# Performance work log

Measured on AMD Instinct MI355X. Metric: run time of the kernel, lower is better.

The kernel has to match this reference:

```python
import jax, jax.numpy as jnp
import numpy as np

# ---- static radial-bin geometry (h == w == 512) ----
H = W = 512
_y, _x = np.indices((H, W))
_center = np.array([(_x.max() - _x.min()) / 2.0, (_y.max() - _y.min()) / 2.0])
_r = np.hypot(_x - _center[0], _y - _center[1])
_r_int = _r.astype(int)
NBINS = int(_r_int.max()) + 1            # all integer radii 0..NBINS-1 are present
R_INT = jnp.asarray(_r_int.ravel())       # (H*W,) int32 bin id per pixel
COUNTS = jnp.asarray(np.bincount(_r_int.ravel(), minlength=NBINS).astype(np.float32))

EPS = 1e-8


def _get_mask(freq_ri):
    """Vectorized equivalent of PSDLoss.get_mask. freq_ri: (n,c,h,w,2).

    azimuthalAverage's sort+cumsum binning == per-integer-radius mean,
    excluding bin 0 and the last bin. The sequential np.where idx-scan in
    psd1D_circle_mask is equivalent to a gather psd_ext[r_int] because psd
    values lie in [0,1] (the only possible collision, value 1.0 at idx=1,
    rewrites bin 0 with psd_ext[1] == psd_ext[0], a no-op).
    """
    comp = (freq_ri[..., 0] + EPS) + 1j * freq_ri[..., 1]   # freq_np += 1e-8
    mag = 20.0 * jnp.log(jnp.abs(comp))                      # magnitude spectrum
    n, c, h, w = mag.shape
    flat = mag.reshape(n, c, h * w)
    seg = lambda m: jax.ops.segment_sum(m, R_INT, num_segments=NBINS)
    sums = jax.vmap(jax.vmap(seg))(flat)                     # (n,c,NBINS)
    binmean = sums / COUNTS
    psd = binmean[..., 1:NBINS - 1]                          # bins 1..NBINS-2
    pmin = psd.min(axis=-1, keepdims=True)
    pmax = psd.max(axis=-1, keepdims=True)
    psd = (psd - pmin) / (pmax - pmin)                       # normalize to [0,1]
    # extend: prepend psd[0], append 0 -> length NBINS, indexed by r_int
    zero = jnp.zeros(psd.shape[:-1] + (1,), psd.dtype)
    psd_ext = jnp.concatenate([psd[..., :1], psd, zero], axis=-1)  # (n,c,NBINS)
    mask = jnp.take(psd_ext, R_INT, axis=-1).reshape(n, c, h, w)
    return mask


def _tensor2freq(img):
    f = jnp.fft.fftshift(jnp.fft.fft2(img), axes=(2, 3))
    return jnp.stack([f.real, f.imag], axis=-1)              # (n,c,h,w,2)


def reference(pred, target):
    loss_weight = 1.0
    pred_freq = _tensor2freq(pred)
    target_freq = _tensor2freq(target)
    # norm='l2', weight='recon', matrix=None (defaults)
    tmp = pred_freq ** 2 - target_freq ** 2
    tmp = tmp[..., 0] + tmp[..., 1]
    freq_distance = tmp ** 2
    mask_all = jax.lax.stop_gradient(_get_mask(pred_freq))   # detached weight
    wmat = 1.0 - mask_all
    wmat = jnp.where(jnp.isnan(wmat), 0.0, wmat)
    wmat = jnp.clip(wmat, 0.0, 1.0)
    return jnp.mean(wmat * freq_distance) * loss_weight


def setup_inputs() -> dict:
    key = jax.random.key(0)
    k1, k2 = jax.random.split(key)
    pred = jax.random.normal(k1, (8, 3, 512, 512), dtype=jnp.float32)
    target = jax.random.normal(k2, (8, 3, 512, 512), dtype=jnp.float32)
    return {"pred": pred, "target": target}
```

## Files before the change

### kernel.cpp

```cpp
#include <hip/hip_runtime.h>
#include <math.h>

#define HW 512
#define NIMG 24
#define NB 362
#define PLANE (HW*HW)
#define NC 257
#define CP (NC*HW)
#define NG 65
#define NPB (NIMG*NG)

#define OFF_PM  0
#define OFF_PD  (NPB*NB)
#define OFF_CNT (2*NPB*NB)
#define OFF_PR  1129808
#define OFF_PIm (OFF_PR + NIMG*CP)
#define OFF_TR  (OFF_PR + 2*NIMG*CP)
#define OFF_TI  (OFF_PR + 3*NIMG*CP)

__device__ __forceinline__ int rbin_odd(float u, float v) {
    return (int)(sqrtf(fmaf(u, u, v*v)) * 0.5f);
}

__device__ __forceinline__ void cmul(float& xr, float& xi, float wr, float wi) {
    float r = xr*wr - xi*wi;
    xi = xr*wi + xi*wr;
    xr = r;
}

__device__ __forceinline__ void dft8(float ar[8], float ai[8]) {
    const float C = 0.70710678118654752440f;
    float t0r=ar[0]+ar[4], t0i=ai[0]+ai[4];
    float t1r=ar[0]-ar[4], t1i=ai[0]-ai[4];
    float t2r=ar[2]+ar[6], t2i=ai[2]+ai[6];
    float t3r=ar[2]-ar[6], t3i=ai[2]-ai[6];
    float E0r=t0r+t2r, E0i=t0i+t2i;
    float E2r=t0r-t2r, E2i=t0i-t2i;
    float E1r=t1r+t3i, E1i=t1i-t3r;
    float E3r=t1r-t3i, E3i=t1i+t3r;
    float u0r=ar[1]+ar[5], u0i=ai[1]+ai[5];
    float u1r=ar[1]-ar[5], u1i=ai[1]-ai[5];
    float u2r=ar[3]+ar[7], u2i=ai[3]+ai[7];
    float u3r=ar[3]-ar[7], u3i=ai[3]-ai[7];
    float O0r=u0r+u2r, O0i=u0i+u2i;
    float O2r=u0r-u2r, O2i=u0i-u2i;
    float O1r=u1r+u3i, O1i=u1i-u3r;
    float O3r=u1r-u3i, O3i=u1i+u3r;
    float W1r = C*(O1r+O1i), W1i = C*(O1i-O1r);
    float W2r = O2i,         W2i = -O2r;
    float W3r = C*(O3i-O3r), W3i = -C*(O3r+O3i);
    ar[0]=E0r+O0r; ai[0]=E0i+O0i;
    ar[4]=E0r-O0r; ai[4]=E0i-O0i;
    ar[1]=E1r+W1r; ai[1]=E1i+W1i;
    ar[5]=E1r-W1r; ai[5]=E1i-W1i;
    ar[2]=E2r+W2r; ai[2]=E2i+W2i;
    ar[6]=E2r-W2r; ai[6]=E2i-W2i;
    ar[3]=E3r+W3r; ai[3]=E3i+W3i;
    ar[7]=E3r-W3r; ai[7]=E3i-W3i;
}

__device__ __forceinline__ void twiddle7(float ar[8], float ai[8], float wr, float wi) {
    float pr = wr, pi = wi;
    cmul(ar[1], ai[1], pr, pi);
    #pragma unroll
    for (int k = 2; k < 8; ++k) {
        float nr = pr*wr - pi*wi;
        pi = pr*wi + pi*wr;
        pr = nr;
        cmul(ar[k], ai[k], pr, pi);
    }
}

__device__ __forceinline__ void fft512x2(float Ar[8], float Ai[8],
                                         float Br[8], float Bi[8],
                                         float* Lr, float* Li, int lane) {
    float s1, c1, s2, c2;
    int k1 = lane >> 3, b = lane & 7;
    __sincosf((float)lane * (-6.28318530717958647692f/512.0f), &s1, &c1);
    __sincosf((float)b    * (-6.28318530717958647692f/64.0f),  &s2, &c2);
    dft8(Ar, Ai); twiddle7(Ar, Ai, c1, s1);
    dft8(Br, Bi); twiddle7(Br, Bi, c1, s1);
    #pragma unroll
    for (int j = 0; j < 8; ++j) { Lr[j*68+lane] = Ar[j]; Li[j*68+lane] = Ai[j]; }
    #pragma unroll
    for (int a = 0; a < 8; ++a) { Ar[a] = Lr[k1*68+8*a+b]; Ai[a] = Li[k1*68+8*a+b]; }
    #pragma unroll
    for (int j = 0; j < 8; ++j) { Lr[j*68+lane] = Br[j]; Li[j*68+lane] = Bi[j]; }
    dft8(Ar, Ai); twiddle7(Ar, Ai, c2, s2);
    #pragma unroll
    for (int a = 0; a < 8; ++a) { Br[a] = Lr[k1*68+8*a+b]; Bi[a] = Li[k1*68+8*a+b]; }
    dft8(Br, Bi); twiddle7(Br, Bi, c2, s2);
    #pragma unroll
    for (int cc = 0; cc < 8; ++cc) {
        int ad = k1*68 + 8*cc + ((b + cc) & 7);
        Lr[ad] = Ar[cc]; Li[ad] = Ai[cc];
    }
    #pragma unroll
    for (int bb = 0; bb < 8; ++bb) {
        int ad = k1*68 + 8*b + ((bb + b) & 7);
        Ar[bb] = Lr[ad]; Ai[bb] = Li[ad];
    }
    #pragma unroll
    for (int cc = 0; cc < 8; ++cc) {
        int ad = k1*68 + 8*cc + ((b + cc) & 7);
        Lr[ad] = Br[cc]; Li[ad] = Bi[cc];
    }
    dft8(Ar, Ai);
    #pragma unroll
    for (int bb = 0; bb < 8; ++bb) {
        int ad = k1*68 + 8*b + ((bb + b) & 7);
        Br[bb] = Lr[ad]; Bi[bb] = Li[ad];
    }
    dft8(Br, Bi);
}

__global__ __launch_bounds__(256) void k_counts(int* __restrict__ counts) {
    __shared__ int cb[NB];
    int t = threadIdx.x;
    for (int j = t; j < NB; j += 256) cb[j] = 0;
    __syncthreads();
    int base = blockIdx.x * 4096;
    #pragma unroll
    for (int j = 0; j < 16; ++j) {
        int idx = base + t + j*256;
        float u = fabsf(2.0f*(float)(idx >> 9)  - 511.0f);
        float v = fabsf(2.0f*(float)(idx & 511) - 511.0f);
        atomicAdd(&cb[rbin_odd(u, v)], 1);
    }
    __syncthreads();
    for (int j = t; j < NB; j += 256) atomicAdd(&counts[j], cb[j]);
}

__global__ __launch_bounds__(256, 6) void k_rowfft(const float* __restrict__ pred,
                                                   const float* __restrict__ tgt,
                                                   float* __restrict__ ws) {
    __shared__ float smem[4672];
    int t = threadIdx.x, lane = t & 63, w = t >> 6;
    int b = blockIdx.x;
    int img = b >> 6;
    int r0 = (b & 63) << 3;
    int rA = r0 + 2*w;
    const float* pA = pred + (size_t)img*PLANE + (size_t)rA*HW;
    const float* tA = tgt  + (size_t)img*PLANE + (size_t)rA*HW;
    float arA[8], aiA[8], arB[8], aiB[8];
    #pragma unroll
    for (int j = 0; j < 8; ++j) {
        arA[j] = pA[64*j + lane];      aiA[j] = tA[64*j + lane];
        arB[j] = pA[HW + 64*j + lane]; aiB[j] = tA[HW + 64*j + lane];
    }
    float* Lr = smem + w*1088;
    float* Li = Lr + 544;
    fft512x2(arA, aiA, arB, aiB, Lr, Li, lane);
    float PrA[4], PiA[4], TrA[4], TiA[4], P256A=0.f, T256A=0.f;
    float PrB[4], PiB[4], TrB[4], TiB[4], P256B=0.f, T256B=0.f;
    #pragma unroll
    for (int d = 0; d < 8; ++d) {
        int k = (lane>>3) + ((lane&7)<<3) + (d<<6);
        Lr[k] = arA[d]; Li[k] = aiA[d];
    }
    #pragma unroll
    for (int m = 0; m < 4; ++m) {
        int kk = 64*m + lane, j2 = (512 - kk) & 511;
        float z1r = Lr[kk], z1i = Li[kk], z2r = Lr[j2], z2i = Li[j2];
        PrA[m] = 0.5f*(z1r+z2r); PiA[m] = 0.5f*(z1i-z2i);
        TrA[m] = 0.5f*(z1i+z2i); TiA[m] = 0.5f*(z2r-z1r);
    }
    if (lane == 0) { P256A = Lr[256]; T256A = Li[256]; }
    #pragma unroll
    for (int d = 0; d < 8; ++d) {
        int k = (lane>>3) + ((lane&7)<<3) + (d<<6);
        Lr[k] = arB[d]; Li[k] = aiB[d];
    }
    #pragma unroll
    for (int m = 0; m < 4; ++m) {
        int kk = 64*m + lane, j2 = (512 - kk) & 511;
        float z1r = Lr[kk], z1i = Li[kk], z2r = Lr[j2], z2i = Li[j2];
        PrB[m] = 0.5f*(z1r+z2r); PiB[m] = 0.5f*(z1i-z2i);
        TrB[m] = 0.5f*(z1i+z2i); TiB[m] = 0.5f*(z2r-z1r);
    }
    if (lane == 0) { P256B = Lr[256]; T256B = Li[256]; }

    float* TAt = smem;
    float* TBt = smem + 2336;
    __syncthreads();
    #pragma unroll
    for (int m = 0; m < 4; ++m) {
        int kk = 64*m + lane;
        TAt[kk*9 + 2*w]   = PrA[m]; TAt[kk*9 + 2*w+1] = PrB[m];
        TBt[kk*9 + 2*w]   = PiA[m]; TBt[kk*9 + 2*w+1] = PiB[m];
    }
    if (lane == 0) {
        TAt[256*9 + 2*w] = P256A; TAt[256*9 + 2*w+1] = P256B;
        TBt[256*9 + 2*w] = 0.f;   TBt[256*9 + 2*w+1] = 0.f;
    }
    __syncthreads();
    for (int idx = t; idx < 2*NC; idx += 256) {
        int comp = (idx >= NC);
        int col = idx - comp*NC;
        const float* Tt = comp ? TBt : TAt;
        float* outP = ws + (size_t)(comp ? OFF_PIm : OFF_PR)
                      + (size_t)img*CP + (size_t)col*HW + r0;
        *(float4*)outP       = make_float4(Tt[col*9],   Tt[col*9+1], Tt[col*9+2], Tt[col*9+3]);
        *(float4*)(outP + 4) = make_float4(Tt[col*9+4], Tt[col*9+5], Tt[col*9+6], Tt[col*9+7]);
    }
    __syncthreads();
    #pragma unroll
    for (int m = 0; m < 4; ++m) {
        int kk = 64*m + lane;
        TAt[kk*9 + 2*w]   = TrA[m]; TAt[kk*9 + 2*w+1] = TrB[m];
        TBt[kk*9 + 2*w]   = TiA[m]; TBt[kk*9 + 2*w+1] = TiB[m];
    }
    if (lane == 0) {
        TAt[256*9 + 2*w] = T256A; TAt[256*9 + 2*w+1] = T256B;
        TBt[256*9 + 2*w] = 0.f;   TBt[256*9 + 2*w+1] = 0.f;
    }
    __syncthreads();
    for (int idx = t; idx < 2*NC; idx += 256) {
        int comp = (idx >= NC);
        int col = idx - comp*NC;
        const float* Tt = comp ? TBt : TAt;
        float* outP = ws + (size_t)(comp ? OFF_TI : OFF_TR)
                      + (size_t)img*CP + (size_t)col*HW + r0;
        *(float4*)outP       = make_float4(Tt[col*9],   Tt[col*9+1], Tt[col*9+2], Tt[col*9+3]);
        *(float4*)(outP + 4) = make_float4(Tt[col*9+4], Tt[col*9+5], Tt[col*9+6], Tt[col*9+7]);
    }
}

__global__ __launch_bounds__(256, 6) void k_colfft(const float* __restrict__ ws,
                                                   float* __restrict__ gPM,
                                                   float* __restrict__ gPD) {
    __shared__ float smem[4352];
    __shared__ float binM[NB], binD[NB];
    int t = threadIdx.x, lane = t & 63, w = t >> 6;
    for (int j = t; j < NB; j += 256) { binM[j] = 0.f; binD[j] = 0.f; }
    __syncthreads();
    int b = blockIdx.x;
    int img = b / NG;
    int g = b - img*NG;
    int c = 4*g + w;
    if (c < NC) {
        float* Lr = smem + w*1088;
        float* Li = Lr + 544;
        float prm[8], pim[8], trm[8], tim[8];
        const float* cPR = ws + OFF_PR  + (size_t)img*CP + (size_t)c*HW;
        const float* cPI = ws + OFF_PIm + (size_t)img*CP + (size_t)c*HW;
        const float* cTR = ws + OFF_TR  + (size_t)img*CP + (size_t)c*HW;
        const float* cTI = ws + OFF_TI  + (size_t)img*CP + (size_t)c*HW;
        #pragma unroll
        for (int j = 0; j < 8; ++j) {
            prm[j] = cPR[64*j+lane]; pim[j] = cPI[64*j+lane];
            trm[j] = cTR[64*j+lane]; tim[j] = cTI[64*j+lane];
        }
        fft512x2(prm, pim, trm, tim, Lr, Li, lane);
        #pragma unroll
        for (int d = 0; d < 8; ++d) {
            int ky = (lane>>3) + ((lane&7)<<3) + (d<<6);
            float sp  = prm[d]*prm[d] + pim[d]*pim[d];
            float st_ = trm[d]*trm[d] + tim[d]*tim[d];
            float diff = sp - st_;
            float er = prm[d] + 1e-8f;
            Lr[ky] = 10.0f * __logf(er*er + pim[d]*pim[d]);
            Li[ky] = diff*diff;
        }
        float v1 = (c == 256) ? 511.0f : (float)(2*c + 1);
        bool mir = (c >= 1 && c <= 255);
        float v2 = (float)(2*c - 1);
        #pragma unroll
        for (int p = 0; p < 4; ++p) {
            int ky = lane + 64*p;
            float u = (float)(2*ky + 1);
            float sM = Lr[ky] + Lr[511 - ky];
            float sD = Li[ky] + Li[511 - ky];
            int k1 = rbin_odd(u, v1);
            atomicAdd(&binM[k1], sM);
            atomicAdd(&binD[k1], sD);
            if (mir) {
                float s2M = Lr[(512 - ky) & 511] + Lr[ky + 1];
                float s2D = Li[(512 - ky) & 511] + Li[ky + 1];
                int k2 = rbin_odd(u, v2);
                atomicAdd(&binM[k2], s2M);
                atomicAdd(&binD[k2], s2D);
            }
        }
    }
    __syncthreads();
    for (int j = t; j < NB; j += 256) {
        gPM[(size_t)b*NB + j] = binM[j];
        gPD[(size_t)b*NB + j] = binD[j];
    }
}

__global__ __launch_bounds__(512) void k_final(const float* __restrict__ gPM,
                                               const float* __restrict__ gPD,
                                               const int* __restrict__ counts,
                                               float* __restrict__ out) {
    __shared__ float meanb[NB];
    __shared__ float dsum[NB];
    __shared__ float rmin[512], rmax[512];
    __shared__ double sred[512];
    int t = threadIdx.x, img = blockIdx.x;
    for (int j = t; j < NB; j += 512) {
        float sm = 0.f, sd = 0.f;
        for (int g = 0; g < NG; ++g) {
            sm += gPM[(size_t)(img*NG + g)*NB + j];
            sd += gPD[(size_t)(img*NG + g)*NB + j];
        }
        meanb[j] = sm / (float)counts[j];
        dsum[j] = sd;
    }
    __syncthreads();
    float vmin = INFINITY, vmax = -INFINITY;
    if (t >= 1 && t <= 360) { vmin = meanb[t]; vmax = meanb[t]; }
    rmin[t] = vmin; rmax[t] = vmax;
    __syncthreads();
    for (int s = 256; s > 0; s >>= 1) {
        if (t < s) {
            float a = rmin[t], bb = rmin[t+s];
            rmin[t] = (a != a || bb != bb) ? __int_as_float(0x7fc00000) : fminf(a, bb);
            a = rmax[t]; bb = rmax[t+s];
            rmax[t] = (a != a || bb != bb) ? __int_as_float(0x7fc00000) : fmaxf(a, bb);
        }
        __syncthreads();
    }
    float pmin = rmin[0], pmax = rmax[0];
    double part = 0.0;
    for (int k = t; k < NB; k += 512) {
        float wgt;
        if (k == NB - 1) {
            wgt = 1.0f;
        } else {
            int idx = (k == 0) ? 1 : k;
            float e = (meanb[idx] - pmin) / (pmax - pmin);
            float wv = 1.0f - e;
            if (wv != wv) wv = 0.0f;
            wv = fminf(fmaxf(wv, 0.0f), 1.0f);
            wgt = wv;
        }
        part += (double)wgt * (double)dsum[k];
    }
    sred[t] = part;
    __syncthreads();
    for (int s = 256; s > 0; s >>= 1) {
        if (t < s) sred[t] += sred[t+s];
        __syncthreads();
    }
    if (t == 0) atomicAdd(out, (float)(sred[0] / 6291456.0));
}

extern "C" void kernel_launch(void* const* d_in, const int* in_sizes, int n_in,
                              void* d_out, int out_size, void* d_ws, size_t ws_size,
                              hipStream_t stream) {
    const float* pred = (const float*)d_in[0];
    const float* tgt  = (const float*)d_in[1];
    float* ws = (float*)d_ws;
    hipMemsetAsync((char*)d_ws + (size_t)OFF_CNT*4, 0, NB*4, stream);
    hipMemsetAsync(d_out, 0, sizeof(float), stream);
    k_counts<<<64, 256, 0, stream>>>((int*)(ws + OFF_CNT));
    k_rowfft<<<NIMG*64, 256, 0, stream>>>(pred, tgt, ws);
    k_colfft<<<NPB, 256, 0, stream>>>(ws, ws + OFF_PM, ws + OFF_PD);
    k_final<<<NIMG, 512, 0, stream>>>(ws + OFF_PM, ws + OFF_PD,
                                      (const int*)(ws + OFF_CNT), (float*)d_out);
}
```

Baseline: 186.5 us.

## Interleave intermediate columns in groups of four and fold bin counts into final kernel

The intermediate spectrum layout changes from column-major planes to groups of four interleaved columns, so the row-FFT kernel writes full float4 rows out of a row-major shared tile instead of strided 8-float column chunks. The column-FFT kernel reads with a stride of four. The separate bin-count kernel and its memset are removed, and each final block now recomputes the per-bin pixel counts from one quadrant in shared memory. Launch-bounds occupancy hints drop from 6 to 4. The change saves two launches and aims for better-coalesced writes, at the cost of strided column reads and redundant count work in every final block.

```diff
diff --git a/kernel.cpp b/kernel.cpp
--- a/kernel.cpp
+++ b/kernel.cpp
@@ -6,17 +6,16 @@
 #define NB 362
 #define PLANE (HW*HW)
 #define NC 257
-#define CP (NC*HW)
 #define NG 65
 #define NPB (NIMG*NG)
+#define CP2 133120
 
 #define OFF_PM  0
 #define OFF_PD  (NPB*NB)
-#define OFF_CNT (2*NPB*NB)
-#define OFF_PR  1129808
-#define OFF_PIm (OFF_PR + NIMG*CP)
-#define OFF_TR  (OFF_PR + 2*NIMG*CP)
-#define OFF_TI  (OFF_PR + 3*NIMG*CP)
+#define OFF_PR  (2*NPB*NB)
+#define OFF_PIm (OFF_PR + NIMG*CP2)
+#define OFF_TR  (OFF_PR + 2*NIMG*CP2)
+#define OFF_TI  (OFF_PR + 3*NIMG*CP2)
 
 __device__ __forceinline__ int rbin_odd(float u, float v) {
     return (int)(sqrtf(fmaf(u, u, v*v)) * 0.5f);
@@ -114,27 +113,10 @@
     dft8(Br, Bi);
 }
 
-__global__ __launch_bounds__(256) void k_counts(int* __restrict__ counts) {
-    __shared__ int cb[NB];
-    int t = threadIdx.x;
-    for (int j = t; j < NB; j += 256) cb[j] = 0;
-    __syncthreads();
-    int base = blockIdx.x * 4096;
-    #pragma unroll
-    for (int j = 0; j < 16; ++j) {
-        int idx = base + t + j*256;
-        float u = fabsf(2.0f*(float)(idx >> 9)  - 511.0f);
-        float v = fabsf(2.0f*(float)(idx & 511) - 511.0f);
-        atomicAdd(&cb[rbin_odd(u, v)], 1);
-    }
-    __syncthreads();
-    for (int j = t; j < NB; j += 256) atomicAdd(&counts[j], cb[j]);
-}
-
-__global__ __launch_bounds__(256, 6) void k_rowfft(const float* __restrict__ pred,
+__global__ __launch_bounds__(256, 4) void k_rowfft(const float* __restrict__ pred,
                                                    const float* __restrict__ tgt,
                                                    float* __restrict__ ws) {
-    __shared__ float smem[4672];
+    __shared__ float smem[4352];
     int t = threadIdx.x, lane = t & 63, w = t >> 6;
     int b = blockIdx.x;
     int img = b >> 6;
@@ -180,53 +162,55 @@
     }
     if (lane == 0) { P256B = Lr[256]; T256B = Li[256]; }
 
-    float* TAt = smem;
-    float* TBt = smem + 2336;
+    float* tR = smem;
+    float* tI = smem + 2080;
     __syncthreads();
     #pragma unroll
     for (int m = 0; m < 4; ++m) {
         int kk = 64*m + lane;
-        TAt[kk*9 + 2*w]   = PrA[m]; TAt[kk*9 + 2*w+1] = PrB[m];
-        TBt[kk*9 + 2*w]   = PiA[m]; TBt[kk*9 + 2*w+1] = PiB[m];
+        tR[(2*w)*260 + kk]   = PrA[m]; tR[(2*w+1)*260 + kk] = PrB[m];
+        tI[(2*w)*260 + kk]   = PiA[m]; tI[(2*w+1)*260 + kk] = PiB[m];
     }
     if (lane == 0) {
-        TAt[256*9 + 2*w] = P256A; TAt[256*9 + 2*w+1] = P256B;
-        TBt[256*9 + 2*w] = 0.f;   TBt[256*9 + 2*w+1] = 0.f;
-    }
-    __syncthreads();
-    for (int idx = t; idx < 2*NC; idx += 256) {
-        int comp = (idx >= NC);
-        int col = idx - comp*NC;
-        const float* Tt = comp ? TBt : TAt;
+        tR[(2*w)*260 + 256] = P256A; tR[(2*w+1)*260 + 256] = P256B;
+        tI[(2*w)*260 + 256] = 0.f;   tI[(2*w+1)*260 + 256] = 0.f;
+    }
+    __syncthreads();
+    for (int idx = t; idx < 1040; idx += 256) {
+        int comp = idx >= 520;
+        int q = idx - (comp ? 520 : 0);
+        int cg = q >> 3, rl = q & 7;
+        const float* Tt = comp ? tI : tR;
+        float4 v = *(const float4*)(Tt + rl*260 + 4*cg);
         float* outP = ws + (size_t)(comp ? OFF_PIm : OFF_PR)
-                      + (size_t)img*CP + (size_t)col*HW + r0;
-        *(float4*)outP       = make_float4(Tt[col*9],   Tt[col*9+1], Tt[col*9+2], Tt[col*9+3]);
-        *(float4*)(outP + 4) = make_float4(Tt[col*9+4], Tt[col*9+5], Tt[col*9+6], Tt[col*9+7]);
+                      + (size_t)img*CP2 + cg*2048 + (r0 + rl)*4;
+        *(float4*)outP = v;
     }
     __syncthreads();
     #pragma unroll
     for (int m = 0; m < 4; ++m) {
         int kk = 64*m + lane;
-        TAt[kk*9 + 2*w]   = TrA[m]; TAt[kk*9 + 2*w+1] = TrB[m];
-        TBt[kk*9 + 2*w]   = TiA[m]; TBt[kk*9 + 2*w+1] = TiB[m];
+        tR[(2*w)*260 + kk]   = TrA[m]; tR[(2*w+1)*260 + kk] = TrB[m];
+        tI[(2*w)*260 + kk]   = TiA[m]; tI[(2*w+1)*260 + kk] = TiB[m];
     }
     if (lane == 0) {
-        TAt[256*9 + 2*w] = T256A; TAt[256*9 + 2*w+1] = T256B;
-        TBt[256*9 + 2*w] = 0.f;   TBt[256*9 + 2*w+1] = 0.f;
-    }
-    __syncthreads();
-    for (int idx = t; idx < 2*NC; idx += 256) {
-        int comp = (idx >= NC);
-        int col = idx - comp*NC;
-        const float* Tt = comp ? TBt : TAt;
+        tR[(2*w)*260 + 256] = T256A; tR[(2*w+1)*260 + 256] = T256B;
+        tI[(2*w)*260 + 256] = 0.f;   tI[(2*w+1)*260 + 256] = 0.f;
+    }
+    __syncthreads();
+    for (int idx = t; idx < 1040; idx += 256) {
+        int comp = idx >= 520;
+        int q = idx - (comp ? 520 : 0);
+        int cg = q >> 3, rl = q & 7;
+        const float* Tt = comp ? tI : tR;
+        float4 v = *(const float4*)(Tt + rl*260 + 4*cg);
         float* outP = ws + (size_t)(comp ? OFF_TI : OFF_TR)
-                      + (size_t)img*CP + (size_t)col*HW + r0;
-        *(float4*)outP       = make_float4(Tt[col*9],   Tt[col*9+1], Tt[col*9+2], Tt[col*9+3]);
-        *(float4*)(outP + 4) = make_float4(Tt[col*9+4], Tt[col*9+5], Tt[col*9+6], Tt[col*9+7]);
-    }
-}
-
-__global__ __launch_bounds__(256, 6) void k_colfft(const float* __restrict__ ws,
+                      + (size_t)img*CP2 + cg*2048 + (r0 + rl)*4;
+        *(float4*)outP = v;
+    }
+}
+
+__global__ __launch_bounds__(256, 4) void k_colfft(const float* __restrict__ ws,
                                                    float* __restrict__ gPM,
                                                    float* __restrict__ gPD) {
     __shared__ float smem[4352];
@@ -242,14 +226,16 @@
         float* Lr = smem + w*1088;
         float* Li = Lr + 544;
         float prm[8], pim[8], trm[8], tim[8];
-        const float* cPR = ws + OFF_PR  + (size_t)img*CP + (size_t)c*HW;
-        const float* cPI = ws + OFF_PIm + (size_t)img*CP + (size_t)c*HW;
-        const float* cTR = ws + OFF_TR  + (size_t)img*CP + (size_t)c*HW;
-        const float* cTI = ws + OFF_TI  + (size_t)img*CP + (size_t)c*HW;
+        size_t cbase = (size_t)img*CP2 + (size_t)(c >> 2)*2048 + (c & 3);
+        const float* cPR = ws + OFF_PR  + cbase;
+        const float* cPI = ws + OFF_PIm + cbase;
+        const float* cTR = ws + OFF_TR  + cbase;
+        const float* cTI = ws + OFF_TI  + cbase;
         #pragma unroll
         for (int j = 0; j < 8; ++j) {
-            prm[j] = cPR[64*j+lane]; pim[j] = cPI[64*j+lane];
-            trm[j] = cTR[64*j+lane]; tim[j] = cTI[64*j+lane];
+            int o = (64*j + lane) << 2;
+            prm[j] = cPR[o]; pim[j] = cPI[o];
+            trm[j] = cTR[o]; tim[j] = cTI[o];
         }
         fft512x2(prm, pim, trm, tim, Lr, Li, lane);
         #pragma unroll
@@ -292,20 +278,28 @@
 
 __global__ __launch_bounds__(512) void k_final(const float* __restrict__ gPM,
                                                const float* __restrict__ gPD,
-                                               const int* __restrict__ counts,
                                                float* __restrict__ out) {
+    __shared__ int cnt[NB];
     __shared__ float meanb[NB];
     __shared__ float dsum[NB];
     __shared__ float rmin[512], rmax[512];
     __shared__ double sred[512];
     int t = threadIdx.x, img = blockIdx.x;
+    for (int j = t; j < NB; j += 512) cnt[j] = 0;
+    __syncthreads();
+    for (int q = t; q < 65536; q += 512) {
+        float u = (float)(2*(q >> 8) + 1);
+        float v = (float)(2*(q & 255) + 1);
+        atomicAdd(&cnt[rbin_odd(u, v)], 4);
+    }
+    __syncthreads();
     for (int j = t; j < NB; j += 512) {
         float sm = 0.f, sd = 0.f;
         for (int g = 0; g < NG; ++g) {
             sm += gPM[(size_t)(img*NG + g)*NB + j];
             sd += gPD[(size_t)(img*NG + g)*NB + j];
         }
-        meanb[j] = sm / (float)counts[j];
+        meanb[j] = sm / (float)cnt[j];
         dsum[j] = sd;
     }
     __syncthreads();
@@ -353,11 +347,8 @@
     const float* pred = (const float*)d_in[0];
     const float* tgt  = (const float*)d_in[1];
     float* ws = (float*)d_ws;
-    hipMemsetAsync((char*)d_ws + (size_t)OFF_CNT*4, 0, NB*4, stream);
     hipMemsetAsync(d_out, 0, sizeof(float), stream);
-    k_counts<<<64, 256, 0, stream>>>((int*)(ws + OFF_CNT));
     k_rowfft<<<NIMG*64, 256, 0, stream>>>(pred, tgt, ws);
     k_colfft<<<NPB, 256, 0, stream>>>(ws, ws + OFF_PM, ws + OFF_PD);
-    k_final<<<NIMG, 512, 0, stream>>>(ws + OFF_PM, ws + OFF_PD,
-                                      (const int*)(ws + OFF_CNT), (float*)d_out);
-}
+    k_final<<<NIMG, 512, 0, stream>>>(ws + OFF_PM, ws + OFF_PD, (float*)d_out);
+}
```

New measurement: 168.1 us. 1.11x faster.
